# Kernel tuning notes

Measured on AMD Instinct MI355X. Metric: run time of the kernel, lower is better.

The kernel has to match this reference:

```python
import jax, jax.numpy as jnp
import numpy as np
from jax import lax

B, C, T = 4, 512, 2304
H = 16
D = C // H          # 32 head dim
WIN = 19            # window_size
WOV = WIN // 2      # window_overlap = 9
W = 2 * WOV + 1     # band width = 19
EPS = 1e-5          # nn.LayerNorm default eps


def _dwconv(x, w):
    # depthwise Conv1d, kernel 3, pad 1, no bias, groups=C. x:[B,C,T], w:[C,1,3]
    return lax.conv_general_dilated(x, w, (1,), ((1, 1),),
                                    dimension_numbers=('NCH', 'OIH', 'NCH'),
                                    feature_group_count=C)


def _ln_c(x, g, b):
    # LayerNorm over channel dim of [B,C,T] (torch: permute->LN(n_embd)->permute)
    m = jnp.mean(x, axis=1, keepdims=True)
    v = jnp.var(x, axis=1, keepdims=True)
    return (x - m) * lax.rsqrt(v + EPS) * g[None, :, None] + b[None, :, None]


def _pw(x, w, b):
    # 1x1 Conv1d: [B,C,T] x [O,C] -> [B,O,T]
    return jnp.einsum('oc,bct->bot', w, x) + b[None, :, None]


def setup_inputs() -> dict:
    key = jax.random.key(0)
    ks = jax.random.split(key, 10)
    s = lambda shape, k, fan: jax.random.normal(k, shape, jnp.float32) * (1.0 / np.sqrt(fan))
    inp = {
        'x': jax.random.normal(ks[0], (B, C, T), jnp.float32),
        'w_qconv': s((C, 1, 3), ks[1], 3),
        'w_kconv': s((C, 1, 3), ks[2], 3),
        'w_vconv': s((C, 1, 3), ks[3], 3),
        'g_q': jnp.ones((C,), jnp.float32), 'b_q': jnp.zeros((C,), jnp.float32),
        'g_k': jnp.ones((C,), jnp.float32), 'b_k': jnp.zeros((C,), jnp.float32),
        'g_v': jnp.ones((C,), jnp.float32), 'b_v': jnp.zeros((C,), jnp.float32),
        'w_query': s((C, C), ks[4], C), 'b_query': jnp.zeros((C,), jnp.float32),
        'w_key': s((C, C), ks[5], C), 'b_key': jnp.zeros((C,), jnp.float32),
        'w_value': s((C, C), ks[6], C), 'b_value': jnp.zeros((C,), jnp.float32),
        'w_proj': s((C, C), ks[7], C), 'b_proj': jnp.zeros((C,), jnp.float32),
    }
    # realistic variable-length padding mask (valid prefix per sequence)
    lengths = jax.random.randint(ks[8], (B,), T // 2, T + 1)
    inp['mask'] = jnp.arange(T)[None, :] < lengths[:, None]  # [B,T] bool
    return inp


def reference(x, mask, w_qconv, w_kconv, w_vconv, g_q, b_q, g_k, b_k, g_v, b_v,
              w_query, b_query, w_key, b_key, w_value, b_value, w_proj, b_proj):
    mf = mask.astype(x.dtype)[:, None, :]  # [B,1,T]
    # depthwise conv QKV (+ mask) -> LayerNorm -> 1x1 projection
    q = _pw(_ln_c(_dwconv(x, w_qconv) * mf, g_q, b_q), w_query, b_query)
    k = _pw(_ln_c(_dwconv(x, w_kconv) * mf, g_k, b_k), w_key, b_key)
    v = _pw(_ln_c(_dwconv(x, w_vconv) * mf, g_v, b_v), w_value, b_value)
    # split heads: [B,C,T] -> [B,H,T,D] (channel layout C = H*D)
    split = lambda t: t.reshape(B, H, D, T).transpose(0, 1, 3, 2)
    q, k, v = split(q), split(k), split(v)
    scale = 1.0 / np.sqrt(D)
    # banded sliding-window attention: key position for (t, j) is t + j - WOV
    idx = jnp.arange(T)[:, None] + jnp.arange(W)[None, :]  # [T,W] indices into padded axis
    pad4 = lambda t: jnp.pad(t, ((0, 0), (0, 0), (WOV, WOV), (0, 0)))
    kg = pad4(k)[:, :, idx, :]  # [B,H,T,W,D]
    vg = pad4(v)[:, :, idx, :]  # [B,H,T,W,D]
    scores = jnp.einsum('bhtd,bhtwd->bhtw', q, kg) * scale  # [B,H,T,W]
    valid = (idx >= WOV) & (idx < T + WOV)  # in-range key positions [T,W]
    keym = jnp.pad(mask, ((0, 0), (WOV, WOV)))[:, idx]  # [B,T,W] kv padding mask
    addm = jnp.where(keym, 0.0, -1e4).astype(x.dtype)[:, None]  # additive -1e4 like torch
    scores = jnp.where(valid[None, None], scores + addm, -jnp.inf)
    probs = jax.nn.softmax(scores, axis=-1)
    probs = jnp.where(mask[:, None, :, None], probs, 0.0)  # zero masked query rows
    out = jnp.einsum('bhtw,bhtwd->bhtd', probs, vg)  # [B,H,T,D]
    out = out.transpose(0, 1, 3, 2).reshape(B, C, T)
    out = _pw(out, w_proj, b_proj) * mf
    return out, mask
```

## Files before the change

### kernel.cpp

```cpp
#include <hip/hip_runtime.h>
#include <hip/hip_bf16.h>
#include <cstdint>
#include <cstddef>

#define TB 4
#define TC 512
#define TT 2304
#define TH 16
#define TD 32
#define TW 19
#define WOVR 9
#define EPSLN 1e-5f
#define SCALE 0.17677669529663687f
#define MTOT (TB * TT)
#define KSZ  512

typedef __attribute__((ext_vector_type(8))) short s16x8;
typedef __attribute__((ext_vector_type(8))) unsigned short u16x8;
typedef __attribute__((ext_vector_type(4))) float f32x4;

__device__ __forceinline__ float bf2f(unsigned short u) {
  union { unsigned int i; float f; } x; x.i = ((unsigned int)u) << 16; return x.f;
}
__device__ __forceinline__ unsigned short f2bf(float f) {
  union { __hip_bfloat16 h; unsigned short u; } c;
  c.h = __float2bfloat16(f);
  return c.u;
}
__device__ __forceinline__ void gload16(const void* g, void* l) {
  __builtin_amdgcn_global_load_lds(
      (const __attribute__((address_space(1))) unsigned int*)g,
      (__attribute__((address_space(3))) unsigned int*)l, 16, 0, 0);
}

__global__ void k_prep(const unsigned char* __restrict__ mraw,
                       const float* __restrict__ wq, const float* __restrict__ wk,
                       const float* __restrict__ wv, const float* __restrict__ wp,
                       unsigned short* __restrict__ Wbf,
                       float* __restrict__ mf, float* __restrict__ out) {
  const int i = blockIdx.x * 256 + threadIdx.x;
  if (i < 4 * TC * TC) {
    const int z = i >> 18, r = i & (TC * TC - 1);
    const float* src = (z == 0) ? wq : (z == 1) ? wk : (z == 2) ? wv : wp;
    Wbf[i] = f2bf(src[r]);
  }
  if (i < TB * TT) {
    const uint32_t w0 = *(const uint32_t*)mraw;
    bool on;
    if (w0 == 1u)                 on = ((const int*)mraw)[i] != 0;
    else if (w0 == 0x01010101u)   on = mraw[i] != 0;
    else                          on = ((const float*)mraw)[i] != 0.0f;
    const float v = on ? 1.0f : 0.0f;
    mf[i] = v;
    out[(size_t)TB * TC * TT + i] = v;
  }
}

__global__ __launch_bounds__(512) void k_conv_ln_t(
    const float* __restrict__ x,
    const float* __restrict__ wq, const float* __restrict__ wk, const float* __restrict__ wv,
    const float* __restrict__ gq, const float* __restrict__ bq,
    const float* __restrict__ gk, const float* __restrict__ bk,
    const float* __restrict__ gv, const float* __restrict__ bv,
    const float* __restrict__ mf, unsigned short* __restrict__ Aall) {
  const int b = blockIdx.y;
  const int t0 = blockIdx.x * 16;
  const int tid = threadIdx.x;
  const int tt = tid & 15, cg = tid >> 4;
  const int tg = t0 + tt;
  const float m = mf[b * TT + tg];
  __shared__ float ps[3][32][16], ps2[3][32][16];
  __shared__ float mean_s[3][16], rstd_s[3][16];

  float s0 = 0.f, s20 = 0.f, s1 = 0.f, s21 = 0.f, s2v = 0.f, s22 = 0.f;
  unsigned int yp0[8], yp1[8], yp2[8];
  #pragma unroll
  for (int i = 0; i < 16; i++) {
    const int c = cg * 16 + i;
    const float* xp = x + ((size_t)(b * TC + c)) * TT + tg;
    const float xm1 = (tg > 0)      ? xp[-1] : 0.f;
    const float x0  = xp[0];
    const float xp1 = (tg < TT - 1) ? xp[1]  : 0.f;
    const float yq = (wq[c*3] * xm1 + wq[c*3+1] * x0 + wq[c*3+2] * xp1) * m;
    const float yk = (wk[c*3] * xm1 + wk[c*3+1] * x0 + wk[c*3+2] * xp1) * m;
    const float yv = (wv[c*3] * xm1 + wv[c*3+1] * x0 + wv[c*3+2] * xp1) * m;
    s0 += yq; s20 += yq * yq;
    s1 += yk; s21 += yk * yk;
    s2v += yv; s22 += yv * yv;
    const unsigned int hq = f2bf(yq), hk = f2bf(yk), hv = f2bf(yv);
    if ((i & 1) == 0) { yp0[i>>1] = hq; yp1[i>>1] = hk; yp2[i>>1] = hv; }
    else { yp0[i>>1] |= hq << 16; yp1[i>>1] |= hk << 16; yp2[i>>1] |= hv << 16; }
  }
  ps[0][cg][tt] = s0; ps2[0][cg][tt] = s20;
  ps[1][cg][tt] = s1; ps2[1][cg][tt] = s21;
  ps[2][cg][tt] = s2v; ps2[2][cg][tt] = s22;
  __syncthreads();
  if (tid < 48) {
    const int z = tid >> 4, tl = tid & 15;
    float su = 0.f, su2 = 0.f;
    #pragma unroll
    for (int g = 0; g < 32; g++) { su += ps[z][g][tl]; su2 += ps2[z][g][tl]; }
    const float mean = su * (1.f / TC);
    const float var  = su2 * (1.f / TC) - mean * mean;
    mean_s[z][tl] = mean;
    rstd_s[z][tl] = rsqrtf(fmaxf(var, 0.f) + EPSLN);
  }
  __syncthreads();

  #pragma unroll
  for (int z = 0; z < 3; z++) {
    const unsigned int* yp = (z == 0) ? yp0 : (z == 1) ? yp1 : yp2;
    const float* gp = (z == 0) ? gq : (z == 1) ? gk : gv;
    const float* bp = (z == 0) ? bq : (z == 1) ? bk : bv;
    const float mean = mean_s[z][tt], rs = rstd_s[z][tt];
    unsigned short tmp[16];
    #pragma unroll
    for (int i = 0; i < 16; i++) {
      const int c = cg * 16 + i;
      const unsigned short hb =
          (unsigned short)((i & 1) ? (yp[i>>1] >> 16) : (yp[i>>1] & 0xffffu));
      tmp[i] = f2bf((bf2f(hb) - mean) * rs * gp[c] + bp[c]);
    }
    unsigned short* oz = Aall + ((size_t)z * MTOT + b * TT + tg) * TC + cg * 16;
    *(u16x8*)(oz)     = *(const u16x8*)(tmp);
    *(u16x8*)(oz + 8) = *(const u16x8*)(tmp + 8);
  }
}

template<int BM, int F32OUT>
__global__ __launch_bounds__(256) void k_gemm_mfma(
    const unsigned short* __restrict__ Abase, const unsigned short* __restrict__ Wbase,
    const float* __restrict__ bq, const float* __restrict__ bk, const float* __restrict__ bv,
    unsigned short* __restrict__ obf, float* __restrict__ of32,
    const float* __restrict__ mf) {
  constexpr int MI = BM / 32;
  constexpr int QA = BM / 64;
  constexpr int WROWS = BM / 2;
  const int z = blockIdx.z;
  const unsigned short* A = Abase + (size_t)z * MTOT * KSZ;
  const unsigned short* W = Wbase + (size_t)z * KSZ * KSZ;
  const float* bias = (z == 0) ? bq : (z == 1) ? bk : bv;
  const int m0 = blockIdx.y * BM;
  const int n0 = blockIdx.x * 128;
  __shared__ __align__(16) unsigned short smem[2 * (BM * 32) + 2 * (128 * 32)];
  const int tid = threadIdx.x;
  const int l = tid & 63, l15 = l & 15, l4 = l >> 4;
  const int wid = tid >> 6, wm = wid >> 1, wn = wid & 1;

  int offA[MI], offB[4];
  #pragma unroll
  for (int i = 0; i < MI; i++) {
    const int ra = wm * WROWS + i * 16 + l15;
    offA[i] = (ra * 4 + (l4 ^ ((ra >> 1) & 3))) * 8;
  }
  #pragma unroll
  for (int j = 0; j < 4; j++) {
    const int rb = wn * 64 + j * 16 + l15;
    offB[j] = (rb * 4 + (l4 ^ ((rb >> 1) & 3))) * 8;
  }

  #define STAGE(buf, kk)                                                     \
    do {                                                                     \
      unsigned short* Ad = smem + (buf) * (BM * 32);                         \
      unsigned short* Bd = smem + 2 * (BM * 32) + (buf) * (128 * 32);        \
      _Pragma("unroll")                                                      \
      for (int q = 0; q < QA; q++) {                                         \
        const int row = q * 64 + (tid >> 2);                                 \
        const int cc = (tid & 3) ^ ((row >> 1) & 3);                         \
        gload16(A + (size_t)(m0 + row) * KSZ + (kk) + cc * 8,                \
                Ad + (q * 256 + tid) * 8);                                   \
      }                                                                      \
      _Pragma("unroll")                                                      \
      for (int q = 0; q < 2; q++) {                                          \
        const int row = q * 64 + (tid >> 2);                                 \
        const int cc = (tid & 3) ^ ((row >> 1) & 3);                         \
        gload16(W + (size_t)(n0 + row) * KSZ + (kk) + cc * 8,                \
                Bd + (q * 256 + tid) * 8);                                   \
      }                                                                      \
    } while (0)

  f32x4 acc[MI][4] = {};
  STAGE(0, 0);
  __syncthreads();
  int cur = 0;
  for (int k0 = 0; k0 < KSZ; k0 += 32) {
    if (k0 + 32 < KSZ) STAGE(cur ^ 1, k0 + 32);
    const unsigned short* Ac = smem + cur * (BM * 32);
    const unsigned short* Bc = smem + 2 * (BM * 32) + cur * (128 * 32);
    s16x8 av[MI], bw[4];
    #pragma unroll
    for (int i = 0; i < MI; i++) av[i] = *(const s16x8*)(Ac + offA[i]);
    #pragma unroll
    for (int j = 0; j < 4; j++)  bw[j] = *(const s16x8*)(Bc + offB[j]);
    #pragma unroll
    for (int mi = 0; mi < MI; mi++)
      #pragma unroll
      for (int nj = 0; nj < 4; nj++)
        acc[mi][nj] = __builtin_amdgcn_mfma_f32_16x16x32_bf16(
            bw[nj], av[mi], acc[mi][nj], 0, 0, 0);
    __syncthreads();
    cur ^= 1;
  }
  #undef STAGE

  if (!F32OUT) {
    unsigned short* O = obf + (size_t)z * MTOT * KSZ;
    #pragma unroll
    for (int nj = 0; nj < 4; nj++) {
      const int ch0 = n0 + wn * 64 + nj * 16 + l4 * 4;
      const float4 bi = *(const float4*)&bias[ch0];
      #pragma unroll
      for (int mi = 0; mi < MI; mi++) {
        const int bt = m0 + wm * WROWS + mi * 16 + l15;
        const float v0 = acc[mi][nj][0] + bi.x;
        const float v1 = acc[mi][nj][1] + bi.y;
        const float v2 = acc[mi][nj][2] + bi.z;
        const float v3 = acc[mi][nj][3] + bi.w;
        uint2 pk;
        pk.x = (uint32_t)f2bf(v0) | ((uint32_t)f2bf(v1) << 16);
        pk.y = (uint32_t)f2bf(v2) | ((uint32_t)f2bf(v3) << 16);
        *(uint2*)&O[(size_t)bt * KSZ + ch0] = pk;
      }
    }
  } else {
    const int bb = m0 / TT;
    const int tl0 = m0 - bb * TT;
    #pragma unroll
    for (int mi = 0; mi < MI; mi++) {
      const int bt = m0 + wm * WROWS + mi * 16 + l15;
      const int tloc = tl0 + wm * WROWS + mi * 16 + l15;
      const float mm = mf[bt];
      #pragma unroll
      for (int nj = 0; nj < 4; nj++) {
        const int ch0 = n0 + wn * 64 + nj * 16 + l4 * 4;
        const float4 bi = *(const float4*)&bias[ch0];
        #pragma unroll
        for (int r = 0; r < 4; r++) {
          const float biv = r == 0 ? bi.x : r == 1 ? bi.y : r == 2 ? bi.z : bi.w;
          of32[((size_t)(bb * TC + ch0 + r)) * TT + tloc] =
              (acc[mi][nj][r] + biv) * mm;
        }
      }
    }
  }
}

#define AROWS (128 + 2 * WOVR)
#define ASTR  36
__global__ __launch_bounds__(256) void k_attn_lds(
    const unsigned short* __restrict__ QKV, const float* __restrict__ mf,
    unsigned short* __restrict__ AO) {
  const int t0 = blockIdx.x * 128;
  const int h = blockIdx.y, b = blockIdx.z;
  const int tid = threadIdx.x;
  const int tloc = tid >> 1, half = tid & 1;
  const size_t SZ = (size_t)MTOT * KSZ;
  const unsigned short* Qp = QKV;
  const unsigned short* Kp = QKV + SZ;
  const unsigned short* Vp = QKV + 2 * SZ;
  __shared__ unsigned short Ks[AROWS * ASTR], Vs[AROWS * ASTR];
  __shared__ float mfs[AROWS];

  for (int idx = tid; idx < 2 * AROWS * 4; idx += 256) {
    const int bufv = idx >= AROWS * 4;
    const int ci = idx - bufv * AROWS * 4;
    const int r = ci >> 2, c = ci & 3;
    const int tk = t0 - WOVR + r;
    const int tkc = tk < 0 ? 0 : (tk >= TT ? TT - 1 : tk);
    const unsigned short* src =
        (bufv ? Vp : Kp) + ((size_t)(b * TT + tkc)) * TC + h * TD + c * 8;
    uint4 v = *(const uint4*)src;
    unsigned short* dst = (bufv ? Vs : Ks) + r * ASTR + c * 8;
    uint2 lo; lo.x = v.x; lo.y = v.y;
    uint2 hi; hi.x = v.z; hi.y = v.w;
    *(uint2*)dst = lo; *(uint2*)(dst + 4) = hi;
  }
  if (tid < AROWS) {
    const int tk = t0 - WOVR + tid;
    mfs[tid] = (tk >= 0 && tk < TT) ? (mf[b * TT + tk] != 0.f ? 0.f : -1e4f)
                                    : -1e30f;
  }
  __syncthreads();

  const int t = t0 + tloc;
  const float qm = mf[b * TT + t];
  float q[16];
  {
    const unsigned short* qr = Qp + ((size_t)(b * TT + t)) * TC + h * TD + half * 16;
    #pragma unroll
    for (int c = 0; c < 2; c++) {
      u16x8 v = *(const u16x8*)(qr + c * 8);
      #pragma unroll
      for (int j = 0; j < 8; j++) q[c * 8 + j] = bf2f(v[j]);
    }
  }
  float e[TW];
  float smax = -3.0e38f;
  #pragma unroll
  for (int j = 0; j < TW; j++) {
    const unsigned short* kr = Ks + (tloc + j) * ASTR + half * 16;
    float acc = 0.f;
    #pragma unroll
    for (int c = 0; c < 4; c++) {
      uint2 w = *(const uint2*)(kr + c * 4);
      acc = fmaf(q[c*4+0], bf2f((unsigned short)(w.x & 0xffffu)), acc);
      acc = fmaf(q[c*4+1], bf2f((unsigned short)(w.x >> 16)), acc);
      acc = fmaf(q[c*4+2], bf2f((unsigned short)(w.y & 0xffffu)), acc);
      acc = fmaf(q[c*4+3], bf2f((unsigned short)(w.y >> 16)), acc);
    }
    acc += __shfl_xor(acc, 1, 64);
    const float sv = acc * SCALE + mfs[tloc + j];
    e[j] = sv;
    smax = fmaxf(smax, sv);
  }
  float den = 0.f;
  #pragma unroll
  for (int j = 0; j < TW; j++) { const float ev = __expf(e[j] - smax); e[j] = ev; den += ev; }
  float o[16] = {};
  #pragma unroll
  for (int j = 0; j < TW; j++) {
    const unsigned short* vr = Vs + (tloc + j) * ASTR + half * 16;
    const float p = e[j];
    #pragma unroll
    for (int c = 0; c < 4; c++) {
      uint2 w = *(const uint2*)(vr + c * 4);
      o[c*4+0] = fmaf(p, bf2f((unsigned short)(w.x & 0xffffu)), o[c*4+0]);
      o[c*4+1] = fmaf(p, bf2f((unsigned short)(w.x >> 16)), o[c*4+1]);
      o[c*4+2] = fmaf(p, bf2f((unsigned short)(w.y & 0xffffu)), o[c*4+2]);
      o[c*4+3] = fmaf(p, bf2f((unsigned short)(w.y >> 16)), o[c*4+3]);
    }
  }
  const float sc = qm / den;
  unsigned short tmp[16];
  #pragma unroll
  for (int i = 0; i < 16; i++) tmp[i] = f2bf(o[i] * sc);
  unsigned short* op = AO + ((size_t)(b * TT + t)) * TC + h * TD + half * 16;
  *(u16x8*)(op)     = *(const u16x8*)(tmp);
  *(u16x8*)(op + 8) = *(const u16x8*)(tmp + 8);
}

extern "C" void kernel_launch(void* const* d_in, const int* in_sizes, int n_in,
                              void* d_out, int out_size, void* d_ws, size_t ws_size,
                              hipStream_t stream) {
  const float* x       = (const float*)d_in[0];
  const float* w_qconv = (const float*)d_in[1];
  const float* w_kconv = (const float*)d_in[2];
  const float* w_vconv = (const float*)d_in[3];
  const float* g_q = (const float*)d_in[4];
  const float* b_q = (const float*)d_in[5];
  const float* g_k = (const float*)d_in[6];
  const float* b_k = (const float*)d_in[7];
  const float* g_v = (const float*)d_in[8];
  const float* b_v = (const float*)d_in[9];
  const float* w_query = (const float*)d_in[10];
  const float* b_query = (const float*)d_in[11];
  const float* w_key   = (const float*)d_in[12];
  const float* b_key   = (const float*)d_in[13];
  const float* w_value = (const float*)d_in[14];
  const float* b_value = (const float*)d_in[15];
  const float* w_proj  = (const float*)d_in[16];
  const float* b_proj  = (const float*)d_in[17];
  const unsigned char* mraw = (const unsigned char*)d_in[18];
  float* out = (float*)d_out;

  uint8_t* w8 = (uint8_t*)d_ws;
  float* mf            = (float*)w8;
  unsigned short* Wbf  = (unsigned short*)(w8 + (1ull << 20));
  unsigned short* Aall = (unsigned short*)(w8 + (4ull << 20));
  unsigned short* QKV  = (unsigned short*)(w8 + (34ull << 20));
  unsigned short* AO   = (unsigned short*)(w8 + (63ull << 20));

  k_prep<<<dim3((4 * TC * TC + 255) / 256), dim3(256), 0, stream>>>(
      mraw, w_query, w_key, w_value, w_proj, Wbf, mf, out);
  k_conv_ln_t<<<dim3(TT / 16, TB), dim3(512), 0, stream>>>(
      x, w_qconv, w_kconv, w_vconv, g_q, b_q, g_k, b_k, g_v, b_v, mf, Aall);
  k_gemm_mfma<256, 0><<<dim3(4, MTOT / 256, 3), dim3(256), 0, stream>>>(
      Aall, Wbf, b_query, b_key, b_value, QKV, nullptr, mf);
  k_attn_lds<<<dim3(TT / 128, TH, TB), dim3(256), 0, stream>>>(QKV, mf, AO);
  k_gemm_mfma<128, 1><<<dim3(4, MTOT / 128, 1), dim3(256), 0, stream>>>(
      AO, Wbf + 3 * TC * TC, b_proj, b_proj, b_proj, nullptr, out, mf);
}
```

Baseline: 110.5 us.

## Triple-buffer GEMM loads with explicit waitcnt and XCD-aware 1D block remap

Rewrites the MFMA GEMM to use a fixed 128x128 tile with a three-stage LDS ring buffer, prefetching two K-steps ahead. The full __syncthreads is replaced by inline s_waitcnt vmcnt/s_barrier, so the next loads stay in flight during the MFMAs. The grid becomes 1D with a remap that interleaves blocks across the 8 XCDs, and global address offsets are precomputed. The QKV GEMM now uses smaller M tiles (128 instead of 256), which gives more blocks but less reuse per block. The hand-written vmcnt counts depend on the exact issue order of the global loads.

```diff
diff --git a/kernel.cpp b/kernel.cpp
--- a/kernel.cpp
+++ b/kernel.cpp
@@ -127,79 +127,83 @@
   }
 }
 
-template<int BM, int F32OUT>
+template<int F32OUT>
 __global__ __launch_bounds__(256) void k_gemm_mfma(
     const unsigned short* __restrict__ Abase, const unsigned short* __restrict__ Wbase,
     const float* __restrict__ bq, const float* __restrict__ bk, const float* __restrict__ bv,
     unsigned short* __restrict__ obf, float* __restrict__ of32,
     const float* __restrict__ mf) {
-  constexpr int MI = BM / 32;
-  constexpr int QA = BM / 64;
-  constexpr int WROWS = BM / 2;
-  const int z = blockIdx.z;
+  const int nw = gridDim.x;
+  int w = blockIdx.x;
+  w = (w & 7) * (nw >> 3) + (w >> 3);
+  const int z = w / 288;
+  const int rem = w - z * 288;
+  const int m0 = (rem >> 2) * 128;
+  const int n0 = (rem & 3) * 128;
+
   const unsigned short* A = Abase + (size_t)z * MTOT * KSZ;
   const unsigned short* W = Wbase + (size_t)z * KSZ * KSZ;
   const float* bias = (z == 0) ? bq : (z == 1) ? bk : bv;
-  const int m0 = blockIdx.y * BM;
-  const int n0 = blockIdx.x * 128;
-  __shared__ __align__(16) unsigned short smem[2 * (BM * 32) + 2 * (128 * 32)];
+
+  __shared__ __align__(16) unsigned short smem[6 * 4096];
   const int tid = threadIdx.x;
   const int l = tid & 63, l15 = l & 15, l4 = l >> 4;
   const int wid = tid >> 6, wm = wid >> 1, wn = wid & 1;
 
-  int offA[MI], offB[4];
-  #pragma unroll
-  for (int i = 0; i < MI; i++) {
-    const int ra = wm * WROWS + i * 16 + l15;
+  const int r0 = tid >> 2;
+  const int c0 = (tid & 3) ^ ((r0 >> 1) & 3);
+  const int r1 = r0 + 64;
+  const int c1 = (tid & 3) ^ ((r1 >> 1) & 3);
+  const size_t gaA0 = (size_t)(m0 + r0) * KSZ + c0 * 8;
+  const size_t gaA1 = (size_t)(m0 + r1) * KSZ + c1 * 8;
+  const size_t gaB0 = (size_t)(n0 + r0) * KSZ + c0 * 8;
+  const size_t gaB1 = (size_t)(n0 + r1) * KSZ + c1 * 8;
+
+  int offA[4], offB[4];
+  #pragma unroll
+  for (int i = 0; i < 4; i++) {
+    const int ra = wm * 64 + i * 16 + l15;
     offA[i] = (ra * 4 + (l4 ^ ((ra >> 1) & 3))) * 8;
-  }
-  #pragma unroll
-  for (int j = 0; j < 4; j++) {
-    const int rb = wn * 64 + j * 16 + l15;
-    offB[j] = (rb * 4 + (l4 ^ ((rb >> 1) & 3))) * 8;
-  }
-
-  #define STAGE(buf, kk)                                                     \
-    do {                                                                     \
-      unsigned short* Ad = smem + (buf) * (BM * 32);                         \
-      unsigned short* Bd = smem + 2 * (BM * 32) + (buf) * (128 * 32);        \
-      _Pragma("unroll")                                                      \
-      for (int q = 0; q < QA; q++) {                                         \
-        const int row = q * 64 + (tid >> 2);                                 \
-        const int cc = (tid & 3) ^ ((row >> 1) & 3);                         \
-        gload16(A + (size_t)(m0 + row) * KSZ + (kk) + cc * 8,                \
-                Ad + (q * 256 + tid) * 8);                                   \
-      }                                                                      \
-      _Pragma("unroll")                                                      \
-      for (int q = 0; q < 2; q++) {                                          \
-        const int row = q * 64 + (tid >> 2);                                 \
-        const int cc = (tid & 3) ^ ((row >> 1) & 3);                         \
-        gload16(W + (size_t)(n0 + row) * KSZ + (kk) + cc * 8,                \
-                Bd + (q * 256 + tid) * 8);                                   \
-      }                                                                      \
+    const int rb = wn * 64 + i * 16 + l15;
+    offB[i] = (rb * 4 + (l4 ^ ((rb >> 1) & 3))) * 8;
+  }
+
+  #define STAGE(buf, kk)                                           \
+    do {                                                           \
+      unsigned short* Ad = smem + (buf) * 4096;                    \
+      unsigned short* Bd = smem + 3 * 4096 + (buf) * 4096;         \
+      gload16(A + gaA0 + (kk), Ad + tid * 8);                      \
+      gload16(A + gaA1 + (kk), Ad + (tid + 256) * 8);              \
+      gload16(W + gaB0 + (kk), Bd + tid * 8);                      \
+      gload16(W + gaB1 + (kk), Bd + (tid + 256) * 8);              \
     } while (0)
 
-  f32x4 acc[MI][4] = {};
+  f32x4 acc[4][4] = {};
   STAGE(0, 0);
-  __syncthreads();
-  int cur = 0;
-  for (int k0 = 0; k0 < KSZ; k0 += 32) {
-    if (k0 + 32 < KSZ) STAGE(cur ^ 1, k0 + 32);
-    const unsigned short* Ac = smem + cur * (BM * 32);
-    const unsigned short* Bc = smem + 2 * (BM * 32) + cur * (128 * 32);
-    s16x8 av[MI], bw[4];
-    #pragma unroll
-    for (int i = 0; i < MI; i++) av[i] = *(const s16x8*)(Ac + offA[i]);
-    #pragma unroll
-    for (int j = 0; j < 4; j++)  bw[j] = *(const s16x8*)(Bc + offB[j]);
-    #pragma unroll
-    for (int mi = 0; mi < MI; mi++)
+  STAGE(1, 32);
+  asm volatile("s_waitcnt vmcnt(4)\ns_barrier" ::: "memory");
+
+  #pragma unroll
+  for (int t = 0; t < 16; ++t) {
+    if (t + 2 < 16) STAGE((t + 2) % 3, (t + 2) * 32);
+    const unsigned short* Ac = smem + (t % 3) * 4096;
+    const unsigned short* Bc = smem + 3 * 4096 + (t % 3) * 4096;
+    s16x8 av[4], bw[4];
+    #pragma unroll
+    for (int i = 0; i < 4; i++) {
+      av[i] = *(const s16x8*)(Ac + offA[i]);
+      bw[i] = *(const s16x8*)(Bc + offB[i]);
+    }
+    #pragma unroll
+    for (int mi = 0; mi < 4; mi++)
       #pragma unroll
       for (int nj = 0; nj < 4; nj++)
         acc[mi][nj] = __builtin_amdgcn_mfma_f32_16x16x32_bf16(
             bw[nj], av[mi], acc[mi][nj], 0, 0, 0);
-    __syncthreads();
-    cur ^= 1;
+    if (t < 14)
+      asm volatile("s_waitcnt vmcnt(4) lgkmcnt(0)\ns_barrier" ::: "memory");
+    else if (t == 14)
+      asm volatile("s_waitcnt vmcnt(0) lgkmcnt(0)\ns_barrier" ::: "memory");
   }
   #undef STAGE
 
@@ -210,15 +214,13 @@
       const int ch0 = n0 + wn * 64 + nj * 16 + l4 * 4;
       const float4 bi = *(const float4*)&bias[ch0];
       #pragma unroll
-      for (int mi = 0; mi < MI; mi++) {
-        const int bt = m0 + wm * WROWS + mi * 16 + l15;
-        const float v0 = acc[mi][nj][0] + bi.x;
-        const float v1 = acc[mi][nj][1] + bi.y;
-        const float v2 = acc[mi][nj][2] + bi.z;
-        const float v3 = acc[mi][nj][3] + bi.w;
+      for (int mi = 0; mi < 4; mi++) {
+        const int bt = m0 + wm * 64 + mi * 16 + l15;
         uint2 pk;
-        pk.x = (uint32_t)f2bf(v0) | ((uint32_t)f2bf(v1) << 16);
-        pk.y = (uint32_t)f2bf(v2) | ((uint32_t)f2bf(v3) << 16);
+        pk.x = (uint32_t)f2bf(acc[mi][nj][0] + bi.x) |
+               ((uint32_t)f2bf(acc[mi][nj][1] + bi.y) << 16);
+        pk.y = (uint32_t)f2bf(acc[mi][nj][2] + bi.z) |
+               ((uint32_t)f2bf(acc[mi][nj][3] + bi.w) << 16);
         *(uint2*)&O[(size_t)bt * KSZ + ch0] = pk;
       }
     }
@@ -226,9 +228,9 @@
     const int bb = m0 / TT;
     const int tl0 = m0 - bb * TT;
     #pragma unroll
-    for (int mi = 0; mi < MI; mi++) {
-      const int bt = m0 + wm * WROWS + mi * 16 + l15;
-      const int tloc = tl0 + wm * WROWS + mi * 16 + l15;
+    for (int mi = 0; mi < 4; mi++) {
+      const int bt = m0 + wm * 64 + mi * 16 + l15;
+      const int tloc = tl0 + wm * 64 + mi * 16 + l15;
       const float mm = mf[bt];
       #pragma unroll
       for (int nj = 0; nj < 4; nj++) {
@@ -374,9 +376,9 @@
       mraw, w_query, w_key, w_value, w_proj, Wbf, mf, out);
   k_conv_ln_t<<<dim3(TT / 16, TB), dim3(512), 0, stream>>>(
       x, w_qconv, w_kconv, w_vconv, g_q, b_q, g_k, b_k, g_v, b_v, mf, Aall);
-  k_gemm_mfma<256, 0><<<dim3(4, MTOT / 256, 3), dim3(256), 0, stream>>>(
+  k_gemm_mfma<0><<<dim3(864), dim3(256), 0, stream>>>(
       Aall, Wbf, b_query, b_key, b_value, QKV, nullptr, mf);
   k_attn_lds<<<dim3(TT / 128, TH, TB), dim3(256), 0, stream>>>(QKV, mf, AO);
-  k_gemm_mfma<128, 1><<<dim3(4, MTOT / 128, 1), dim3(256), 0, stream>>>(
+  k_gemm_mfma<1><<<dim3(288), dim3(256), 0, stream>>>(
       AO, Wbf + 3 * TC * TC, b_proj, b_proj, b_proj, nullptr, out, mf);
 }
```

After: 99.19 us. 10.3% less time.
